# Kernel optimization log

Hardware: AMD Instinct MI355X
Metric: run time of the kernel (lower is better)

## Reference

```python
import jax, jax.numpy as jnp
import numpy as np

M, N = 4096, 4096
N_COEF = 768
ALPHA = 16.0


def _dct_mat(K):
    # Orthonormal DCT-II matrix D: D[k, t] = s(k) * cos(pi * (t + 0.5) * k / K)
    # dct2d(X)  = D_M @ X @ D_N.T ;  idct2d(Y) = D_M.T @ Y @ D_N  (DCT-III)
    k = jnp.arange(K, dtype=jnp.float32)[:, None]
    t = jnp.arange(K, dtype=jnp.float32)[None, :]
    D = jnp.cos(jnp.pi * (t + 0.5) * k / K)
    scale = jnp.where(k == 0, jnp.sqrt(1.0 / K), jnp.sqrt(2.0 / K))
    return (D * scale).astype(jnp.float32)


def setup_inputs() -> dict:
    key = jax.random.key(0)
    k1, k2, k3 = jax.random.split(key, 3)
    weight = jax.random.normal(k1, (M, N), dtype=jnp.float32) * 0.02
    dW_params = jax.random.normal(k2, (N_COEF,), dtype=jnp.float32) * 0.05
    flat_indices = jax.random.randint(k3, (N_COEF,), 0, M * N, dtype=jnp.int64)
    return {"weight": weight, "dW_params": dW_params, "flat_indices": flat_indices}


def reference(weight, dW_params, flat_indices):
    # W_eff = stop_grad(W) + idct2d(scatter(dW_params)) * alpha
    m, n = weight.shape
    dW_F = jnp.zeros(m * n, dtype=jnp.float32).at[flat_indices].set(dW_params)
    dW_F = dW_F.reshape(m, n)
    D_M = _dct_mat(m)
    D_N = _dct_mat(n)
    dW_T = D_M.T @ dW_F @ D_N  # dense 2D inverse DCT (DCT-III)
    return jax.lax.stop_gradient(weight) + dW_T * ALPHA
```

## Files before the change

### kernel.cpp

```cpp
#include <hip/hip_runtime.h>

#define MDIM 4096
#define NDIM 4096
#define NCOEF 768
#define ALPHA 16.0f
#define PANEL_I8 (12 * 16384)

typedef __attribute__((ext_vector_type(4))) int   i32x4;
typedef __attribute__((ext_vector_type(4))) float f32x4;

__device__ __forceinline__ void glds16c(const char* src, char* dst) {
    __builtin_amdgcn_global_load_lds(
        (const __attribute__((address_space(1))) void*)src,
        (__attribute__((address_space(3))) void*)dst, 16, 0, 0);
}

__global__ __launch_bounds__(256) void fill_uv(
    const int* __restrict__ fidx, const float* __restrict__ dw,
    char* __restrict__ U8, char* __restrict__ V8, float* __restrict__ csp)
{
    __shared__ int idx_s[NCOEF];
    __shared__ float red[4];
    __shared__ int dup[16];
    __shared__ float su_l[16], sv_l[16];
    const int b = blockIdx.x;
    const int panel = b / 48;
    const int rem = b - panel * 48;
    const int kt = rem >> 2;
    const int k16 = rem & 3;
    const int p0 = kt * 64 + (k16 << 4);
    const int t = threadIdx.x;
    float m = 0.0f;
    #pragma unroll
    for (int j = 0; j < 3; ++j) {
        idx_s[t + (j << 8)] = fidx[t + (j << 8)];
        m = fmaxf(m, fabsf(dw[t + (j << 8)]));
    }
    if (t < 16) dup[t] = 0;
    #pragma unroll
    for (int off = 32; off > 0; off >>= 1) m = fmaxf(m, __shfl_xor(m, off));
    if ((t & 63) == 0) red[t >> 6] = m;
    __syncthreads();
    const float maxdw = fmaxf(fmaxf(red[0], red[1]), fmaxf(red[2], red[3]));
    {
        const int ci = t >> 4;
        const int pci = p0 + ci;
        const int myidx = idx_s[pci];
        const int q0 = (t & 15) * 48;
        int found = 0;
        #pragma unroll
        for (int s = 0; s < 48; ++s) {
            const int q = q0 + s;
            found |= (q > pci) & (idx_s[q] == myidx);
        }
        if (found) dup[ci] = 1;
    }
    __syncthreads();
    const float s0 = 0.015625f;
    const float s1 = 0.022097086912079612f;
    const float Vmax = ALPHA * maxdw * s1;
    const float isV = (Vmax > 0.0f) ? (127.0f / Vmax) : 0.0f;
    if (t < 16) {
        const int p = p0 + t;
        const int idx = idx_s[p];
        const int r = idx >> 12;
        const int c = idx & (NDIM - 1);
        su_l[t] = ((r == 0) ? s0 : s1) * (127.0f / s1);
        sv_l[t] = (dup[t] ? 0.0f : 1.0f) * ALPHA * dw[p] * ((c == 0) ? s0 : s1) * isV;
    }
    if (b == 0 && t == 0) csp[0] = (s1 / 127.0f) * (Vmax / 127.0f);
    __syncthreads();
    const unsigned tt = 2u * (unsigned)((panel << 8) + t) + 1u;
    const float wrev = 1.0f / 16384.0f;
    unsigned wu[4] = {0, 0, 0, 0}, wv[4] = {0, 0, 0, 0};
    #pragma unroll
    for (int j = 0; j < 16; ++j) {
        const int idx = idx_s[p0 + j];
        const unsigned nu = (tt * (unsigned)(idx >> 12)) & 16383u;
        const unsigned nv = (tt * (unsigned)(idx & (NDIM - 1))) & 16383u;
        const int qu = (int)rintf(su_l[j] * __builtin_amdgcn_cosf((float)nu * wrev));
        const int qv = (int)rintf(sv_l[j] * __builtin_amdgcn_cosf((float)nv * wrev));
        wu[j >> 2] |= (unsigned)(qu & 255) << ((j & 3) * 8);
        wv[j >> 2] |= (unsigned)(qv & 255) << ((j & 3) * 8);
    }
    const size_t off = ((size_t)(panel * 12 + kt) * 1024 + (size_t)(k16 << 8) + t) << 4;
    *(uint4*)(U8 + off) = make_uint4(wu[0], wu[1], wu[2], wu[3]);
    *(uint4*)(V8 + off) = make_uint4(wv[0], wv[1], wv[2], wv[3]);
}

__global__ __launch_bounds__(512, 1) void gemm_kernel(
    const float* __restrict__ W,
    const char* __restrict__ U8,
    const char* __restrict__ V8,
    const float* __restrict__ csp,
    float* __restrict__ out)
{
    __shared__ char SM[148992];
    char* const As = SM;
    char* const Bs = SM + 65536;
    float* const L = (float*)(SM + 98304);

    const int tid = threadIdx.x;
    const int lane = tid & 63;
    const int wave = tid >> 6;

    const int bid = blockIdx.x;
    const int xcd = bid & 7;
    const int local = bid >> 3;
    const int by = ((xcd >> 1) << 2) + (local >> 3);
    const int bxp = ((xcd & 1) << 3) + (local & 7);
    const int wr = wave >> 2;
    const int wc = wave & 3;
    const int fr = lane & 15;
    const int fks = lane >> 4;

    const char* uPan = U8 + (size_t)by * PANEL_I8;
    const char* vPanBase = V8 + (size_t)bxp * PANEL_I8;
    const float CS = *csp;

    i32x4 accA[8][2] = {};
    i32x4 accB[8][2] = {};
    float4 wreg[2][2];

    const int aO = (fks << 12) + ((wr * 128 + fr) << 4);
    const int bO = (fks << 11) + (((wc << 5) + fr) << 4);

    const int erowBase = by << 8;
    const int bcolA = bxp << 8;
    const int bcolB = bcolA + 128;
    const int c4 = (tid & 31) << 2;
    const int rsub = tid >> 5;

#define STAGE(s) do {                                                        \
        const int jA = (s) % 12;                                             \
        const char* uS = uPan + ((size_t)jA << 14);                          \
        char* aD = As + (((s) & 3) << 14) + (wave << 10);                    \
        glds16c(uS + (tid << 4), aD);                                        \
        glds16c(uS + 8192 + (tid << 4), aD + 8192);                          \
        const char* vS = vPanBase + ((size_t)jA << 14) + ((tid >> 7) << 12)  \
                         + (((s) >= 12) ? 2048 : 0) + ((tid & 127) << 4);    \
        glds16c(vS, Bs + (((s) & 3) << 13) + (wave << 10));                  \
    } while (0)

#define COMPUTE(buf, ACC) do {                                               \
        i32x4 a[8], b[2];                                                    \
        _Pragma("unroll")                                                    \
        for (int fm = 0; fm < 8; ++fm)                                       \
            a[fm] = *(const i32x4*)(As + (buf) * 16384 + aO + fm * 256);     \
        _Pragma("unroll")                                                    \
        for (int fn = 0; fn < 2; ++fn)                                       \
            b[fn] = *(const i32x4*)(Bs + (buf) * 8192 + bO + fn * 256);      \
        _Pragma("unroll")                                                    \
        for (int fm = 0; fm < 8; ++fm)                                       \
            _Pragma("unroll")                                                \
            for (int fn = 0; fn < 2; ++fn)                                   \
                ACC[fm][fn] = __builtin_amdgcn_mfma_i32_16x16x64_i8(         \
                    b[fn], a[fm], ACC[fm][fn], 0, 0, 0);                     \
    } while (0)

#define LWRITE(C, R, ACC) do {                                               \
        if (wr == ((C) >> 2)) {                                              \
            _Pragma("unroll")                                                \
            for (int f2 = 0; f2 < 2; ++f2)                                   \
                _Pragma("unroll")                                            \
                for (int fn = 0; fn < 2; ++fn) {                             \
                    f32x4 v;                                                 \
                    _Pragma("unroll")                                        \
                    for (int jj = 0; jj < 4; ++jj)                           \
                        v[jj] = CS * (float)ACC[((C) & 3) * 2 + f2][fn][jj]; \
                    *(f32x4*)(L + (R) * 4224 + (f2 * 16 + fr) * 132          \
                              + (wc << 5) + fn * 16 + (fks << 2)) = v;       \
                }                                                            \
        }                                                                    \
    } while (0)

#define WLOAD(C, SLOT, BCOL) do {                                            \
        _Pragma("unroll")                                                    \
        for (int i2 = 0; i2 < 2; ++i2)                                       \
            wreg[SLOT][i2] = *(const float4*)(W                              \
                + (size_t)(erowBase + (C) * 32 + i2 * 16 + rsub) * NDIM      \
                + (BCOL) + c4);                                              \
    } while (0)

#define STORE(C, R, SLOT, BCOL) do {                                         \
        _Pragma("unroll")                                                    \
        for (int i2 = 0; i2 < 2; ++i2) {                                     \
            const int rl = i2 * 16 + rsub;                                   \
            const size_t o = (size_t)(erowBase + (C) * 32 + rl) * NDIM       \
                             + (BCOL) + c4;                                  \
            const f32x4 l4 = *(const f32x4*)(L + (R) * 4224 + rl * 132 + c4);\
            float4 r4;                                                       \
            r4.x = wreg[SLOT][i2].x + l4[0];                                 \
            r4.y = wreg[SLOT][i2].y + l4[1];                                 \
            r4.z = wreg[SLOT][i2].z + l4[2];                                 \
            r4.w = wreg[SLOT][i2].w + l4[3];                                 \
            *(float4*)(out + o) = r4;                                        \
        }                                                                    \
    } while (0)

#define VW(n) asm volatile("s_waitcnt vmcnt(" #n ")" ::: "memory")

#define ITER(I, NC_, NW_, ACC) do {                                          \
        if ((I) <= 21) STAGE((I) + 2);                                       \
        if ((I) >= 12 && (I) <= 19) {                                        \
            LWRITE((I) - 12, ((I) - 12) % 3, accA);                          \
            WLOAD((I) - 12, ((I) - 12) & 1, bcolA);                          \
        }                                                                    \
        VW(NC_);                                                             \
        asm volatile("s_waitcnt lgkmcnt(0)" ::: "memory");                   \
        __builtin_amdgcn_s_barrier();                                        \
        asm volatile("" ::: "memory");                                       \
        COMPUTE((I) & 3, ACC);                                               \
        if ((I) >= 13 && (I) <= 20) {                                        \
            VW(NW_);                                                         \
            STORE((I) - 13, ((I) - 13) % 3, ((I) - 13) & 1, bcolA);          \
        }                                                                    \
    } while (0)

    STAGE(0); STAGE(1);
    ITER(0, 6, 0, accA);  ITER(1, 6, 0, accA);  ITER(2, 6, 0, accA);
    ITER(3, 6, 0, accA);  ITER(4, 6, 0, accA);  ITER(5, 6, 0, accA);
    ITER(6, 6, 0, accA);  ITER(7, 6, 0, accA);  ITER(8, 6, 0, accA);
    ITER(9, 6, 0, accA);  ITER(10, 6, 0, accA); ITER(11, 6, 0, accA);
    ITER(12, 8, 0, accB); ITER(13, 10, 5, accB); ITER(14, 14, 7, accB);
    ITER(15, 16, 7, accB); ITER(16, 16, 7, accB); ITER(17, 16, 7, accB);
    ITER(18, 16, 7, accB); ITER(19, 16, 7, accB); ITER(20, 14, 5, accB);
    ITER(21, 12, 5, accB); ITER(22, 5, 0, accB); ITER(23, 0, 0, accB);

    WLOAD(0, 0, bcolB);
    LWRITE(0, 0, accB);
    #pragma unroll
    for (int c = 0; c < 8; ++c) {
        __syncthreads();
        if (c < 7) {
            WLOAD(c + 1, (c + 1) & 1, bcolB);
            LWRITE(c + 1, (c + 1) & 1, accB);
        }
        STORE(c, c & 1, c & 1, bcolB);
    }
#undef STAGE
#undef COMPUTE
#undef LWRITE
#undef WLOAD
#undef STORE
#undef VW
#undef ITER
}

extern "C" void kernel_launch(void* const* d_in, const int* in_sizes, int n_in,
                              void* d_out, int out_size, void* d_ws, size_t ws_size,
                              hipStream_t stream) {
    const float* weight = (const float*)d_in[0];
    const float* dw     = (const float*)d_in[1];
    const int*   fidx   = (const int*)d_in[2];
    float* out = (float*)d_out;

    char* ws = (char*)d_ws;
    char* U8 = ws;
    char* V8 = ws + 3145728;
    float* csp = (float*)(ws + 2 * 3145728);

    fill_uv<<<16 * 48, 256, 0, stream>>>(fidx, dw, U8, V8, csp);
    gemm_kernel<<<256, 512, 0, stream>>>(weight, U8, V8, csp, out);
}
```

Baseline: 46.05 us.

## Warp-specialize GEMM: half the waves compute while the other half stage and store

```diff
diff --git a/kernel.cpp b/kernel.cpp
--- a/kernel.cpp
+++ b/kernel.cpp
@@ -103,148 +103,222 @@
     const int tid = threadIdx.x;
     const int lane = tid & 63;
     const int wave = tid >> 6;
+    const bool isA = wave < 4;
+    const int wl = wave & 3;
+    const int wr = (wave >> 1) & 1;
+    const int wc = wave & 1;
+    const int fr = lane & 15;
+    const int fks = lane >> 4;
 
     const int bid = blockIdx.x;
     const int xcd = bid & 7;
     const int local = bid >> 3;
     const int by = ((xcd >> 1) << 2) + (local >> 3);
     const int bxp = ((xcd & 1) << 3) + (local & 7);
-    const int wr = wave >> 2;
-    const int wc = wave & 3;
-    const int fr = lane & 15;
-    const int fks = lane >> 4;
 
     const char* uPan = U8 + (size_t)by * PANEL_I8;
-    const char* vPanBase = V8 + (size_t)bxp * PANEL_I8;
+    const char* vPan = V8 + (size_t)bxp * PANEL_I8;
     const float CS = *csp;
 
-    i32x4 accA[8][2] = {};
-    i32x4 accB[8][2] = {};
-    float4 wreg[2][2];
+    i32x4 acc[8][4] = {};
+    f32x4 wregA[2][4];
+    f32x4 wregB[2][2];
 
     const int aO = (fks << 12) + ((wr * 128 + fr) << 4);
-    const int bO = (fks << 11) + (((wc << 5) + fr) << 4);
-
-    const int erowBase = by << 8;
+    const int bO = (fks << 11) + ((wc * 64 + fr) << 4);
+
+    const int erow = by << 8;
     const int bcolA = bxp << 8;
     const int bcolB = bcolA + 128;
-    const int c4 = (tid & 31) << 2;
-    const int rsub = tid >> 5;
-
-#define STAGE(s) do {                                                        \
-        const int jA = (s) % 12;                                             \
-        const char* uS = uPan + ((size_t)jA << 14);                          \
-        char* aD = As + (((s) & 3) << 14) + (wave << 10);                    \
-        glds16c(uS + (tid << 4), aD);                                        \
-        glds16c(uS + 8192 + (tid << 4), aD + 8192);                          \
-        const char* vS = vPanBase + ((size_t)jA << 14) + ((tid >> 7) << 12)  \
-                         + (((s) >= 12) ? 2048 : 0) + ((tid & 127) << 4);    \
-        glds16c(vS, Bs + (((s) & 3) << 13) + (wave << 10));                  \
-    } while (0)
-
-#define COMPUTE(buf, ACC) do {                                               \
-        i32x4 a[8], b[2];                                                    \
+
+#define VWAIT(n) asm volatile("s_waitcnt vmcnt(" #n ")" ::: "memory")
+#define LGKM()   asm volatile("s_waitcnt lgkmcnt(0)" ::: "memory")
+#define BARR()   do { __builtin_amdgcn_s_barrier(); asm volatile("" ::: "memory"); } while (0)
+
+#define STAGE_AB(s) do {                                                     \
+        const char* uS = uPan + (size_t)((s) % 12) * 16384;                  \
+        char* aD = As + ((s) & 3) * 16384 + (wl << 10);                      \
+        glds16c(uS + (wl << 10) + (lane << 4),               aD);            \
+        glds16c(uS + 4096 + (wl << 10) + (lane << 4),        aD + 4096);     \
+        glds16c(uS + 8192 + (wl << 10) + (lane << 4),        aD + 8192);     \
+        glds16c(uS + 12288 + (wl << 10) + (lane << 4),       aD + 12288);    \
+        const char* vS = vPan + (size_t)((s) % 12) * 16384 + ((s) / 12) * 2048; \
+        char* bD = Bs + ((s) & 3) * 8192 + (wl << 10);                       \
+        glds16c(vS + (((wl >> 1) + 0) << 12) + ((wl & 1) << 10) + (lane << 4), bD); \
+        glds16c(vS + (((wl >> 1) + 2) << 12) + ((wl & 1) << 10) + (lane << 4), bD + 4096); \
+    } while (0)
+
+#define COMPUTE(buf) do {                                                    \
+        i32x4 a[8], b[4];                                                    \
         _Pragma("unroll")                                                    \
         for (int fm = 0; fm < 8; ++fm)                                       \
             a[fm] = *(const i32x4*)(As + (buf) * 16384 + aO + fm * 256);     \
         _Pragma("unroll")                                                    \
-        for (int fn = 0; fn < 2; ++fn)                                       \
+        for (int fn = 0; fn < 4; ++fn)                                       \
             b[fn] = *(const i32x4*)(Bs + (buf) * 8192 + bO + fn * 256);      \
         _Pragma("unroll")                                                    \
         for (int fm = 0; fm < 8; ++fm)                                       \
             _Pragma("unroll")                                                \
-            for (int fn = 0; fn < 2; ++fn)                                   \
-                ACC[fm][fn] = __builtin_amdgcn_mfma_i32_16x16x64_i8(         \
-                    b[fn], a[fm], ACC[fm][fn], 0, 0, 0);                     \
-    } while (0)
-
-#define LWRITE(C, R, ACC) do {                                               \
-        if (wr == ((C) >> 2)) {                                              \
+            for (int fn = 0; fn < 4; ++fn)                                   \
+                acc[fm][fn] = __builtin_amdgcn_mfma_i32_16x16x64_i8(         \
+                    b[fn], a[fm], acc[fm][fn], 0, 0, 0);                     \
+    } while (0)
+
+#define WLA(c) do {                                                          \
+        _Pragma("unroll")                                                    \
+        for (int i = 0; i < 4; ++i) {                                        \
+            const int e = i * 256 + tid;                                     \
+            wregA[(c) & 1][i] = __builtin_nontemporal_load((const f32x4*)(   \
+                W + (size_t)(erow + (c) * 32 + (e >> 5)) * NDIM              \
+                  + bcolA + ((e & 31) << 2)));                               \
+        }                                                                    \
+    } while (0)
+#define LWRA(c) do {                                                         \
+        if (wr == ((c) >> 2)) {                                              \
             _Pragma("unroll")                                                \
             for (int f2 = 0; f2 < 2; ++f2)                                   \
                 _Pragma("unroll")                                            \
-                for (int fn = 0; fn < 2; ++fn) {                             \
+                for (int fn = 0; fn < 4; ++fn) {                             \
                     f32x4 v;                                                 \
                     _Pragma("unroll")                                        \
                     for (int jj = 0; jj < 4; ++jj)                           \
-                        v[jj] = CS * (float)ACC[((C) & 3) * 2 + f2][fn][jj]; \
-                    *(f32x4*)(L + (R) * 4224 + (f2 * 16 + fr) * 132          \
-                              + (wc << 5) + fn * 16 + (fks << 2)) = v;       \
+                        v[jj] = CS * (float)acc[((c) & 3) * 2 + f2][fn][jj]; \
+                    *(f32x4*)(L + ((c) % 3) * 4224 + (f2 * 16 + fr) * 132    \
+                              + (wc << 6) + fn * 16 + (fks << 2)) = v;       \
                 }                                                            \
         }                                                                    \
     } while (0)
-
-#define WLOAD(C, SLOT, BCOL) do {                                            \
-        _Pragma("unroll")                                                    \
-        for (int i2 = 0; i2 < 2; ++i2)                                       \
-            wreg[SLOT][i2] = *(const float4*)(W                              \
-                + (size_t)(erowBase + (C) * 32 + i2 * 16 + rsub) * NDIM      \
-                + (BCOL) + c4);                                              \
-    } while (0)
-
-#define STORE(C, R, SLOT, BCOL) do {                                         \
-        _Pragma("unroll")                                                    \
-        for (int i2 = 0; i2 < 2; ++i2) {                                     \
-            const int rl = i2 * 16 + rsub;                                   \
-            const size_t o = (size_t)(erowBase + (C) * 32 + rl) * NDIM       \
-                             + (BCOL) + c4;                                  \
-            const f32x4 l4 = *(const f32x4*)(L + (R) * 4224 + rl * 132 + c4);\
-            float4 r4;                                                       \
-            r4.x = wreg[SLOT][i2].x + l4[0];                                 \
-            r4.y = wreg[SLOT][i2].y + l4[1];                                 \
-            r4.z = wreg[SLOT][i2].z + l4[2];                                 \
-            r4.w = wreg[SLOT][i2].w + l4[3];                                 \
-            *(float4*)(out + o) = r4;                                        \
-        }                                                                    \
-    } while (0)
-
-#define VW(n) asm volatile("s_waitcnt vmcnt(" #n ")" ::: "memory")
-
-#define ITER(I, NC_, NW_, ACC) do {                                          \
-        if ((I) <= 21) STAGE((I) + 2);                                       \
-        if ((I) >= 12 && (I) <= 19) {                                        \
-            LWRITE((I) - 12, ((I) - 12) % 3, accA);                          \
-            WLOAD((I) - 12, ((I) - 12) & 1, bcolA);                          \
-        }                                                                    \
-        VW(NC_);                                                             \
-        asm volatile("s_waitcnt lgkmcnt(0)" ::: "memory");                   \
-        __builtin_amdgcn_s_barrier();                                        \
-        asm volatile("" ::: "memory");                                       \
-        COMPUTE((I) & 3, ACC);                                               \
-        if ((I) >= 13 && (I) <= 20) {                                        \
-            VW(NW_);                                                         \
-            STORE((I) - 13, ((I) - 13) % 3, ((I) - 13) & 1, bcolA);          \
-        }                                                                    \
-    } while (0)
-
-    STAGE(0); STAGE(1);
-    ITER(0, 6, 0, accA);  ITER(1, 6, 0, accA);  ITER(2, 6, 0, accA);
-    ITER(3, 6, 0, accA);  ITER(4, 6, 0, accA);  ITER(5, 6, 0, accA);
-    ITER(6, 6, 0, accA);  ITER(7, 6, 0, accA);  ITER(8, 6, 0, accA);
-    ITER(9, 6, 0, accA);  ITER(10, 6, 0, accA); ITER(11, 6, 0, accA);
-    ITER(12, 8, 0, accB); ITER(13, 10, 5, accB); ITER(14, 14, 7, accB);
-    ITER(15, 16, 7, accB); ITER(16, 16, 7, accB); ITER(17, 16, 7, accB);
-    ITER(18, 16, 7, accB); ITER(19, 16, 7, accB); ITER(20, 14, 5, accB);
-    ITER(21, 12, 5, accB); ITER(22, 5, 0, accB); ITER(23, 0, 0, accB);
-
-    WLOAD(0, 0, bcolB);
-    LWRITE(0, 0, accB);
-    #pragma unroll
-    for (int c = 0; c < 8; ++c) {
-        __syncthreads();
-        if (c < 7) {
-            WLOAD(c + 1, (c + 1) & 1, bcolB);
-            LWRITE(c + 1, (c + 1) & 1, accB);
-        }
-        STORE(c, c & 1, c & 1, bcolB);
-    }
-#undef STAGE
+#define STA(c) do {                                                          \
+        _Pragma("unroll")                                                    \
+        for (int i = 0; i < 4; ++i) {                                        \
+            const int e = i * 256 + tid;                                     \
+            const int rl = e >> 5;                                           \
+            const int cg = e & 31;                                           \
+            const f32x4 l4 = *(const f32x4*)(L + ((c) % 3) * 4224            \
+                                             + rl * 132 + (cg << 2));        \
+            f32x4 r4 = wregA[(c) & 1][i] + l4;                               \
+            __builtin_nontemporal_store(r4, (f32x4*)(                        \
+                out + (size_t)(erow + (c) * 32 + rl) * NDIM                  \
+                    + bcolA + (cg << 2)));                                   \
+        }                                                                    \
+    } while (0)
+
+#define WLB(c) do {                                                          \
+        _Pragma("unroll")                                                    \
+        for (int i = 0; i < 2; ++i) {                                        \
+            const int e = i * 512 + tid;                                     \
+            wregB[(c) & 1][i] = __builtin_nontemporal_load((const f32x4*)(   \
+                W + (size_t)(erow + (c) * 32 + (e >> 5)) * NDIM              \
+                  + bcolB + ((e & 31) << 2)));                               \
+        }                                                                    \
+    } while (0)
+#define LWRB(c) do {                                                         \
+        if (!isA && wr == ((c) >> 2)) {                                      \
+            _Pragma("unroll")                                                \
+            for (int f2 = 0; f2 < 2; ++f2)                                   \
+                _Pragma("unroll")                                            \
+                for (int fn = 0; fn < 4; ++fn) {                             \
+                    f32x4 v;                                                 \
+                    _Pragma("unroll")                                        \
+                    for (int jj = 0; jj < 4; ++jj)                           \
+                        v[jj] = CS * (float)acc[((c) & 3) * 2 + f2][fn][jj]; \
+                    *(f32x4*)(L + ((c) & 1) * 4224 + (f2 * 16 + fr) * 132    \
+                              + (wc << 6) + fn * 16 + (fks << 2)) = v;       \
+                }                                                            \
+        }                                                                    \
+    } while (0)
+#define STB(c) do {                                                          \
+        _Pragma("unroll")                                                    \
+        for (int i = 0; i < 2; ++i) {                                        \
+            const int e = i * 512 + tid;                                     \
+            const int rl = e >> 5;                                           \
+            const int cg = e & 31;                                           \
+            const f32x4 l4 = *(const f32x4*)(L + ((c) & 1) * 4224            \
+                                             + rl * 132 + (cg << 2));        \
+            f32x4 r4 = wregB[(c) & 1][i] + l4;                               \
+            __builtin_nontemporal_store(r4, (f32x4*)(                        \
+                out + (size_t)(erow + (c) * 32 + rl) * NDIM                  \
+                    + bcolB + ((cg) << 2)));                                 \
+        }                                                                    \
+    } while (0)
+
+    if (!isA) { STAGE_AB(0); STAGE_AB(1); VWAIT(6); }
+    LGKM(); BARR();
+
+#define P1(j) do {                                                           \
+        if (!isA) { STAGE_AB((j) + 2); VWAIT(12); }                          \
+        LGKM(); BARR();                                                      \
+        if (isA) COMPUTE((j) & 3);                                           \
+    } while (0)
+    P1(0); P1(1); P1(2); P1(3); P1(4); P1(5);
+    P1(6); P1(7); P1(8); P1(9); P1(10); P1(11);
+
+    if (isA) { WLA(0); STAGE_AB(14); LWRA(0); } else { VWAIT(6); }
+    LGKM(); BARR();
+    if (!isA) COMPUTE(0);
+
+    if (isA) { WLA(1); STAGE_AB(15); LWRA(1); VWAIT(16); } else { VWAIT(0); }
+    LGKM(); BARR();
+    if (!isA) COMPUTE(1);
+    if (isA) STA(0);
+
+#define P2(i, c) do {                                                        \
+        if (isA) { WLA(c); STAGE_AB((i) + 2); LWRA(c); VWAIT(20); }          \
+        LGKM(); BARR();                                                      \
+        if (!isA) COMPUTE((i) & 3);                                          \
+        if (isA) STA((c) - 1);                                               \
+    } while (0)
+    P2(14, 2); P2(15, 3); P2(16, 4); P2(17, 5); P2(18, 6); P2(19, 7);
+
+    if (isA) { STAGE_AB(22); VWAIT(16); }
+    LGKM(); BARR();
+    if (!isA) COMPUTE(0);
+    if (isA) STA(7);
+
+    if (isA) { STAGE_AB(23); VWAIT(20); }
+    LGKM(); BARR();
+    if (!isA) COMPUTE(1);
+
+    if (isA) { VWAIT(10); }
+    LGKM(); BARR();
+    if (!isA) COMPUTE(2);
+
+    if (isA) { VWAIT(0); }
+    LGKM(); BARR();
+    if (!isA) COMPUTE(3);
+
+    WLB(0);
+    LWRB(0);
+    LGKM(); BARR();
+    WLB(1); LWRB(1); VWAIT(2); STB(0);
+    LGKM(); BARR();
+    WLB(2); LWRB(2); VWAIT(4); STB(1);
+    LGKM(); BARR();
+    WLB(3); LWRB(3); VWAIT(4); STB(2);
+    LGKM(); BARR();
+    WLB(4); LWRB(4); VWAIT(4); STB(3);
+    LGKM(); BARR();
+    WLB(5); LWRB(5); VWAIT(4); STB(4);
+    LGKM(); BARR();
+    WLB(6); LWRB(6); VWAIT(4); STB(5);
+    LGKM(); BARR();
+    WLB(7); LWRB(7); VWAIT(4); STB(6);
+    LGKM(); BARR();
+    VWAIT(2); STB(7);
+
+#undef VWAIT
+#undef LGKM
+#undef BARR
+#undef STAGE_AB
 #undef COMPUTE
-#undef LWRITE
-#undef WLOAD
-#undef STORE
-#undef VW
-#undef ITER
+#undef WLA
+#undef LWRA
+#undef STA
+#undef WLB
+#undef LWRB
+#undef STB
+#undef P1
+#undef P2
 }
 
 extern "C" void kernel_launch(void* const* d_in, const int* in_sizes, int n_in,
```

Result: slower. 47.21 us (median of 2 runs) (+2.5%).
